# Performance work log

Hardware: AMD Instinct MI355X
Metric: run time of the kernel (lower is better)

## Reference

```python
import jax, jax.numpy as jnp
import numpy as np

H = 128  # hidden_size


def _cell(x_t, h, c, wih, whh, b):
    # PyTorch LSTM gate order: i, f, g, o
    z = x_t @ wih.T + h @ whh.T + b
    i, f, g, o = jnp.split(z, 4, axis=-1)
    c_new = jax.nn.sigmoid(f) * c + jax.nn.sigmoid(i) * jnp.tanh(g)
    h_new = jax.nn.sigmoid(o) * jnp.tanh(c_new)
    return h_new, c_new


def _layer(xs, wih_f, whh_f, b_f, wih_b, whh_b, b_b):
    # NOTE: faithful to the original per-timestep loop: both 'directions'
    # are stepped FORWARD in time (the backward cell never sees reversed input
    # because each nn.LSTM call has seq_len=1 with carried state).
    B = xs.shape[1]
    init = (jnp.zeros((B, H), xs.dtype), jnp.zeros((B, H), xs.dtype),
            jnp.zeros((B, H), xs.dtype), jnp.zeros((B, H), xs.dtype))

    def step(carry, x_t):
        hf, cf, hb, cb = carry
        hf, cf = _cell(x_t, hf, cf, wih_f, whh_f, b_f)
        hb, cb = _cell(x_t, hb, cb, wih_b, whh_b, b_b)
        return (hf, cf, hb, cb), jnp.concatenate([hf, hb], axis=-1)

    _, ys = jax.lax.scan(step, init, xs)
    return ys  # [S, B, 2H]


def setup_inputs() -> dict:
    key = jax.random.key(0)
    ks = jax.random.split(key, 16)
    S, B, D = 4096, 64, 96
    s = 0.05
    p = {
        'x': jax.random.normal(ks[0], (S, B, D), jnp.float32),
        # layer 0 (input D), forward + backward direction weights
        'wih0f': jax.random.normal(ks[1], (4 * H, D)) * s,
        'whh0f': jax.random.normal(ks[2], (4 * H, H)) * s,
        'b0f': jax.random.normal(ks[3], (4 * H,)) * s,
        'wih0b': jax.random.normal(ks[4], (4 * H, D)) * s,
        'whh0b': jax.random.normal(ks[5], (4 * H, H)) * s,
        'b0b': jax.random.normal(ks[6], (4 * H,)) * s,
        # layer 1 (input 2H)
        'wih1f': jax.random.normal(ks[7], (4 * H, 2 * H)) * s,
        'whh1f': jax.random.normal(ks[8], (4 * H, H)) * s,
        'b1f': jax.random.normal(ks[9], (4 * H,)) * s,
        'wih1b': jax.random.normal(ks[10], (4 * H, 2 * H)) * s,
        'whh1b': jax.random.normal(ks[11], (4 * H, H)) * s,
        'b1b': jax.random.normal(ks[12], (4 * H,)) * s,
        'fc_w': jax.random.normal(ks[13], (1, 2 * H)) * s,
        'fc_b': jax.random.normal(ks[14], (1,)) * s,
    }
    return p


def reference(x, wih0f, whh0f, b0f, wih0b, whh0b, b0b,
              wih1f, whh1f, b1f, wih1b, whh1b, b1b, fc_w, fc_b):
    ys = _layer(x, wih0f, whh0f, b0f, wih0b, whh0b, b0b)      # [S,B,2H]
    ys = _layer(ys, wih1f, whh1f, b1f, wih1b, whh1b, b1b)     # [S,B,2H]
    out = jax.nn.sigmoid(ys @ fc_w.T + fc_b)                  # [S,B,1]
    return out
```

## Files before the change

kernel.cpp:

```cpp
#include <hip/hip_runtime.h>
#include <stdint.h>

typedef short short8 __attribute__((ext_vector_type(8)));
typedef short short4v __attribute__((ext_vector_type(4)));
typedef float floatx4 __attribute__((ext_vector_type(4)));

#define LOG2E 1.44269504088896340736f

template <int N> struct IC { static constexpr int value = N; };

__device__ __forceinline__ float bf2f(unsigned short u) {
  unsigned v = ((unsigned)u) << 16;
  return __builtin_bit_cast(float, v);
}
__device__ __forceinline__ unsigned short f2bf(float f) {
  unsigned v = __builtin_bit_cast(unsigned, f);
  v += 0x7FFFu + ((v >> 16) & 1u);
  return (unsigned short)(v >> 16);
}
__device__ __forceinline__ float fast_exp2(float x) {
#if __has_builtin(__builtin_amdgcn_exp2f)
  return __builtin_amdgcn_exp2f(x);
#else
  return exp2f(x);
#endif
}
__device__ __forceinline__ float fast_rcp(float x) {
#if __has_builtin(__builtin_amdgcn_rcpf)
  return __builtin_amdgcn_rcpf(x);
#else
  return 1.0f / x;
#endif
}
__device__ __forceinline__ float fsig(float x) {
  return fast_rcp(1.0f + fast_exp2(-LOG2E * x));
}
__device__ __forceinline__ floatx4 mfma16(short8 a, short8 b, floatx4 c) {
  return __builtin_amdgcn_mfma_f32_16x16x32_bf16(a, b, c, 0, 0, 0);
}

__global__ __launch_bounds__(256) void detect_kernel(
    const unsigned short* __restrict__ w, int n_u16, int* __restrict__ flag)
{
  __shared__ int cnt;
  if (threadIdx.x == 0) cnt = 0;
  __syncthreads();
  int local = 0;
  for (int i = threadIdx.x * 2; i < n_u16; i += 512) {
    unsigned e = (w[i] >> 7) & 0xFF;
    if (e >= 0xF0) local++;
  }
  atomicAdd(&cnt, local);
  __syncthreads();
  if (threadIdx.x == 0) *flag = (cnt > 64) ? 1 : 0;
}

__global__ __launch_bounds__(256) void convertw_kernel(
    const void* s0, const void* s1, const void* s2, const void* s3,
    const void* s4, const void* s5, const void* s6, const void* s7,
    const void* s8, const void* s9, const void* s10, const void* s11,
    const void* s12, const void* s13,
    unsigned short* __restrict__ wbuf, const int* __restrict__ flag)
{
  const void* srcs[14] = {s0, s1, s2, s3, s4, s5, s6, s7, s8, s9, s10, s11, s12, s13};
  const int woff[14] = {0,      49152,  114688, 115200, 164352, 229888,
                        230400, 361472, 427008, 427520, 558592, 624128,
                        624640, 624896};
  const int wlen[14] = {49152, 65536, 512, 49152, 65536, 512,
                        131072, 65536, 512, 131072, 65536, 512, 256, 1};
  const int glen[14] = {96 * 128, 128 * 128, 128, 96 * 128, 128 * 128, 128,
                        256 * 128, 128 * 128, 128, 256 * 128, 128 * 128, 128,
                        0, 0};
  int sb = 0, i = 0;
  for (i = 0; i < 14; ++i) {
    int nb = (wlen[i] + 1023) >> 10;
    if ((int)blockIdx.x < sb + nb) break;
    sb += nb;
  }
  const int base = ((int)blockIdx.x - sb) * 1024 + (int)threadIdx.x * 4;
  unsigned short* dst = wbuf + woff[i];
  const int f32 = *flag;
  const int gl = glen[i];
#pragma unroll
  for (int j = 0; j < 4; ++j) {
    const int idx = base + j;
    if (idx >= wlen[i]) break;
    float v = f32 ? ((const float*)srcs[i])[idx]
                  : bf2f(((const unsigned short*)srcs[i])[idx]);
    if (gl) {
      const int gate = (int)((unsigned)idx / (unsigned)gl);
      v *= (gate == 2) ? (2.0f * LOG2E) : LOG2E;
    }
    dst[idx] = f2bf(v);
  }
}

template <int K>
__device__ __forceinline__ void gemm512_body(
    unsigned short* As, int t, int slice,
    const void* __restrict__ A, size_t a_off, int dyn,
    const int* __restrict__ flag,
    const unsigned short* __restrict__ Bf, const unsigned short* __restrict__ Bb,
    const unsigned short* __restrict__ biasf, const unsigned short* __restrict__ biasb,
    unsigned short* __restrict__ Z)
{
  constexpr int RS = K + 8;
  const int tid = threadIdx.x, lane = tid & 63;
  const int q = lane >> 4, cc = lane & 15;
  constexpr int K8 = K / 8;
  const int use32 = dyn ? *flag : 0;
  if (use32) {
    const float* Arow = (const float*)A + a_off + (size_t)t * 64 * K;
    for (int ci = tid; ci < 64 * K8; ci += 512) {
      int r_ = ci / K8, c8 = ci % K8;
      const float* p = Arow + r_ * K + c8 * 8;
      floatx4 x0 = *(const floatx4*)p;
      floatx4 x1 = *(const floatx4*)(p + 4);
      short8 s;
#pragma unroll
      for (int j = 0; j < 4; ++j) {
        s[j] = (short)f2bf(x0[j]);
        s[4 + j] = (short)f2bf(x1[j]);
      }
      *(short8*)&As[r_ * RS + c8 * 8] = s;
    }
  } else {
    const unsigned short* Arow = (const unsigned short*)A + a_off + (size_t)t * 64 * K;
    for (int ci = tid; ci < 64 * K8; ci += 512) {
      int r_ = ci / K8, c8 = ci % K8;
      *(short8*)&As[r_ * RS + c8 * 8] = *(const short8*)&Arow[r_ * K + c8 * 8];
    }
  }
  __syncthreads();
  const int w = tid >> 6;
  const unsigned short* Bp    = slice ? Bb : Bf;
  const unsigned short* biasp = slice ? biasb : biasf;
  const int cb = w * 64;
  const int dslab = slice * 4;
  floatx4 acc[4][4];
#pragma unroll
  for (int m = 0; m < 4; ++m)
#pragma unroll
    for (int n = 0; n < 4; ++n)
#pragma unroll
      for (int r = 0; r < 4; ++r) acc[m][n][r] = 0.f;
#pragma unroll
  for (int ks = 0; ks < K / 32; ++ks) {
    short8 af[4], bfr[4];
#pragma unroll
    for (int m = 0; m < 4; ++m)
      af[m] = *(const short8*)&As[(m * 16 + cc) * RS + ks * 32 + q * 8];
#pragma unroll
    for (int n = 0; n < 4; ++n)
      bfr[n] = *(const short8*)&Bp[(size_t)(cb + n * 16 + cc) * K + ks * 32 + q * 8];
#pragma unroll
    for (int m = 0; m < 4; ++m)
#pragma unroll
      for (int n = 0; n < 4; ++n)
        acc[m][n] = mfma16(af[m], bfr[n], acc[m][n]);
  }
#pragma unroll
  for (int n = 0; n < 4; ++n) {
    const int col = cb + n * 16 + cc;
    const float bv = bf2f(biasp[col]);
    const int g = col >> 7, uu = col & 127;
#pragma unroll
    for (int m = 0; m < 4; ++m) {
      unsigned short* zb =
          Z + ((size_t)t * 8 + dslab + m) * 8192 + uu * 16 + q * 4 + g;
#pragma unroll
      for (int r = 0; r < 4; ++r)
        zb[r * 2048] = f2bf(acc[m][n][r] + bv);
    }
  }
}

__device__ __forceinline__ void fc512_body(
    int idx, int steps, const unsigned short* __restrict__ ys1,
    const unsigned short* __restrict__ fcw, const unsigned short* __restrict__ fcb,
    void* __restrict__ out, size_t out_off, const int* __restrict__ flag)
{
  const int tid = threadIdx.x;
  const int w = tid >> 6, lane = tid & 63;
  const int t = idx * 2 + (w >> 2);
  if (t >= steps) return;
  const int w4 = w & 3;
  const int o = lane & 15, q = lane >> 4;
  const int b = w4 * 16 + o;
  const unsigned short* rp = ys1 + ((size_t)t * 64 + b) * 256 + q * 64;
  float s = 0.f;
#pragma unroll
  for (int j = 0; j < 16; ++j) {
    short4v v = *(const short4v*)(rp + j * 4);
    const unsigned short* wp = fcw + q * 64 + j * 4;
#pragma unroll
    for (int k = 0; k < 4; ++k) s += bf2f((unsigned short)v[k]) * bf2f(wp[k]);
  }
  s += __shfl_xor(s, 16, 64);
  s += __shfl_xor(s, 32, 64);
  if (q == 0) {
    const float v = fsig(s + bf2f(fcb[0]));
    const size_t oidx = out_off + (size_t)t * 64 + b;
    if (*flag) ((float*)out)[oidx] = v;
    else       ((unsigned short*)out)[oidx] = f2bf(v);
  }
}

__global__ __attribute__((amdgpu_waves_per_eu(2, 4))) __launch_bounds__(512)
void rec_kernel(
    const unsigned short* __restrict__ Za, const unsigned short* __restrict__ whhfa,
    const unsigned short* __restrict__ whhba,
    unsigned short* __restrict__ ysa, float* __restrict__ ca,
    unsigned short* __restrict__ ha, int inita, int acta,
    const unsigned short* __restrict__ Zb, const unsigned short* __restrict__ whhfb,
    const unsigned short* __restrict__ whhbb,
    unsigned short* __restrict__ ysb, float* __restrict__ cb_,
    unsigned short* __restrict__ hb, int initb, int actb,
    int steps,
    const void* __restrict__ x, size_t x_off, int do96, const int* __restrict__ flag,
    const unsigned short* __restrict__ wih0f, const unsigned short* __restrict__ wih0b,
    const unsigned short* __restrict__ b0f, const unsigned short* __restrict__ b0b,
    unsigned short* __restrict__ Z0n,
    const unsigned short* __restrict__ ys0g, int do256,
    const unsigned short* __restrict__ wih1f, const unsigned short* __restrict__ wih1b,
    const unsigned short* __restrict__ b1f, const unsigned short* __restrict__ b1b,
    unsigned short* __restrict__ Z1n,
    const unsigned short* __restrict__ fcsrc,
    const unsigned short* __restrict__ fcw, const unsigned short* __restrict__ fcb,
    void* __restrict__ out, size_t fc_off, int fcn)
{
  __shared__ __align__(16) unsigned char smem[34816];
  const int bx = blockIdx.x;
  const int g96n = steps * 2;

  if (bx >= 64) {
    const int wi = bx - 64;
    if (wi < g96n) {
      if (!do96) return;
      gemm512_body<96>((unsigned short*)smem, wi >> 1, wi & 1, x, x_off, 1,
                       flag, wih0f, wih0b, b0f, b0b, Z0n);
    } else if (wi < 2 * g96n) {
      if (!do256) return;
      const int idx = wi - g96n;
      gemm512_body<256>((unsigned short*)smem, idx >> 1, idx & 1, ys0g, 0, 0,
                        flag, wih1f, wih1b, b1f, b1b, Z1n);
    } else {
      if (fcn <= 0) return;
      fc512_body(wi - 2 * g96n, steps, fcsrc, fcw, fcb, out, fc_off, flag);
    }
    return;
  }

  const int blk = bx;
  const int ctx = blk >> 5;
  if (ctx == 0 ? !acta : !actb) return;
  const int tid = threadIdx.x;

  const unsigned short* Z;
  const unsigned short* whhF;
  const unsigned short* whhB;
  unsigned short* ys;
  float* cst;
  unsigned short* hst;
  int init;
  if (ctx == 0) {
    Z = Za; whhF = whhfa; whhB = whhba; ys = ysa; cst = ca; hst = ha; init = inita;
  } else {
    Z = Zb; whhF = whhfb; whhB = whhbb; ys = ysb; cst = cb_; hst = hb; init = initb;
  }
  const int d = (blk >> 4) & 1, bg = (blk >> 2) & 3, bh = blk & 3;
  const unsigned short* whh = d ? whhB : whhF;

  unsigned short (*hbuf)[16][136] = (unsigned short(*)[16][136])smem;

  const int w = tid >> 6, lane = tid & 63, q = lane >> 4, cc = lane & 15;
  const int u = w * 16 + cc;

  short8 bfrag[4][4];
#pragma unroll
  for (int g = 0; g < 4; ++g)
#pragma unroll
    for (int k = 0; k < 4; ++k)
      bfrag[g][k] = *(const short8*)(whh + (size_t)(g * 128 + u) * 128 + k * 32 + q * 8);

  const int prow = (tid >> 7) * 4 + bh;
  const int pcol = tid & 127;

  {
    unsigned* hz = (unsigned*)smem;
    for (int i = tid; i < 2 * 16 * 68; i += 512) hz[i] = 0u;
  }
  __syncthreads();

  float creg;
  if (init) {
    creg = 0.f;
  } else {
    creg = cst[(size_t)(d * 64 + bg * 16 + q * 4 + bh) * 128 + u];
    hbuf[0][prow][pcol] = hst[(size_t)(d * 64 + bg * 16 + prow) * 128 + pcol];
  }
  __syncthreads();

  const size_t zoff =
      (size_t)(d * 4 + bg) * 8192 + (size_t)bh * 2048 + u * 16 + q * 4;
  const unsigned short* zpA = Z + zoff;
  const unsigned short* zpB = Z + zoff + 65536;
  short4v zA = *(const short4v*)zpA;
  short4v zB = *(const short4v*)zpB;
  zpA += 131072;
  zpB += 131072;

  unsigned short* ysb_ = ys + (size_t)(bg * 16 + prow) * 256 + d * 128 + pcol;

  auto half_step = [&](auto bhc, short4v& zs, const unsigned short*& zp, int t,
                       int cur, int nxt) __attribute__((always_inline)) {
    constexpr int BH = decltype(bhc)::value;
    floatx4 acc[4];
#pragma unroll
    for (int g = 0; g < 4; ++g)
#pragma unroll
      for (int r = 0; r < 4; ++r)
        acc[g][r] = (r == BH) ? bf2f((unsigned short)zs[g]) : 0.f;
    zs = *(const short4v*)zp;
    zp += 131072;

    short8 af[4];
#pragma unroll
    for (int k = 0; k < 4; ++k)
      af[k] = *(const short8*)&hbuf[cur][cc][k * 32 + q * 8];
#pragma unroll
    for (int g = 0; g < 4; ++g)
#pragma unroll
      for (int k = 0; k < 4; ++k)
        acc[g] = mfma16(af[k], bfrag[g][k], acc[g]);

    {
      const float ei = fast_exp2(acc[0][BH]);
      const float ef = fast_exp2(acc[1][BH]);
      const float eg = fast_exp2(acc[2][BH]);
      const float a1 = 1.0f + ei, a2 = 1.0f + eg, a3 = 1.0f + ef;
      const float p12 = a1 * a2;
      const float rD = fast_rcp(p12 * a3);
      const float t2 = __builtin_fmaf(eg, 2.0f * LOG2E, -2.0f * LOG2E);
      const float it2 = ei * t2 * (a3 * rD);
      const float sf = ef * (p12 * rD);
      const float cs = __builtin_fmaf(sf, creg, it2);
      creg = cs;
      const float eo = fast_exp2(acc[3][BH]);
      const float ec = fast_exp2(fminf(cs, 88.0f));
      const float h = eo * (ec - 1.0f) * fast_rcp((1.0f + eo) * (1.0f + ec));
      hbuf[nxt][q * 4 + BH][u] = f2bf(h);
    }
    asm volatile("s_waitcnt lgkmcnt(0)\n\ts_barrier" ::: "memory");
    ysb_[(size_t)t * 16384] = hbuf[nxt][prow][pcol];
  };

  auto run = [&](auto bhc) __attribute__((always_inline)) {
    int t = 0;
    for (; t + 2 <= steps; t += 2) {
      half_step(bhc, zA, zpA, t, 0, 1);
      half_step(bhc, zB, zpB, t + 1, 1, 0);
    }
    if (t < steps)
      half_step(bhc, zA, zpA, t, 0, 1);
  };
  switch (bh) {
    case 0: run(IC<0>{}); break;
    case 1: run(IC<1>{}); break;
    case 2: run(IC<2>{}); break;
    default: run(IC<3>{}); break;
  }

  cst[(size_t)(d * 64 + bg * 16 + q * 4 + bh) * 128 + u] = creg;
  const int fin = steps & 1;
  hst[(size_t)(d * 64 + bg * 16 + prow) * 128 + pcol] = hbuf[fin][prow][pcol];
}

__global__ __attribute__((amdgpu_waves_per_eu(2, 4))) __launch_bounds__(512)
void g96_kernel(
    const void* __restrict__ x, size_t x_off, const int* __restrict__ flag,
    const unsigned short* __restrict__ Bf, const unsigned short* __restrict__ Bb,
    const unsigned short* __restrict__ biasf, const unsigned short* __restrict__ biasb,
    unsigned short* __restrict__ Z)
{
  __shared__ __align__(16) unsigned short As[64 * 104];
  gemm512_body<96>(As, blockIdx.x >> 1, blockIdx.x & 1, x, x_off, 1, flag,
                   Bf, Bb, biasf, biasb, Z);
}

__global__ __launch_bounds__(256) void fc_kernel(
    const unsigned short* __restrict__ ys,
    const unsigned short* __restrict__ fcw,
    const unsigned short* __restrict__ fcb,
    void* __restrict__ out, size_t out_off, int n,
    const int* __restrict__ flag)
{
  const int gw = (int)((blockIdx.x * 256 + threadIdx.x) >> 6);
  const int lane = threadIdx.x & 63;
  if (gw >= n) return;
  const unsigned short* rp = ys + (size_t)gw * 256 + lane * 4;
  float s = 0.f;
#pragma unroll
  for (int i = 0; i < 4; ++i) s += bf2f(rp[i]) * bf2f(fcw[lane * 4 + i]);
#pragma unroll
  for (int m = 32; m >= 1; m >>= 1) s += __shfl_xor(s, m, 64);
  if (lane == 0) {
    const float v = fsig(s + bf2f(fcb[0]));
    if (*flag) ((float*)out)[out_off + gw] = v;
    else       ((unsigned short*)out)[out_off + gw] = f2bf(v);
  }
}

extern "C" void kernel_launch(void* const* d_in, const int* in_sizes, int n_in,
                              void* d_out, int out_size, void* d_ws, size_t ws_size,
                              hipStream_t stream)
{
  (void)in_sizes; (void)n_in; (void)out_size;
  const int S = 4096;

  int* flag = (int*)d_ws;
  unsigned short* wbuf = (unsigned short*)((char*)d_ws + 256);
  static const int woff[14] = {0,      49152,  114688, 115200, 164352, 229888,
                               230400, 361472, 427008, 427520, 558592, 624128,
                               624640, 624896};
  const size_t wbuf_end = 256 + 1250304;

  int C = 1;
  for (int cand = 128; cand >= 1; cand >>= 1) {
    size_t need = (size_t)cand * 655360 + wbuf_end + 196608;
    if (need <= ws_size) { C = cand; break; }
  }
  unsigned short* base = (unsigned short*)((char*)d_ws + wbuf_end);
  unsigned short* Z0buf[2] = {base, base + (size_t)C * 65536};
  unsigned short* Z1buf[2] = {base + (size_t)2 * C * 65536, base + (size_t)3 * C * 65536};
  unsigned short* ys0buf[2] = {base + (size_t)4 * C * 65536,
                               base + (size_t)4 * C * 65536 + (size_t)C * 16384};
  unsigned short* ys1buf[2] = {base + (size_t)4 * C * 65536 + (size_t)2 * C * 16384,
                               base + (size_t)4 * C * 65536 + (size_t)3 * C * 16384};
  float* c0 = (float*)(base + (size_t)4 * C * 65536 + (size_t)4 * C * 16384);
  float* c1 = c0 + 16384;
  unsigned short* h0 = (unsigned short*)(c1 + 16384);
  unsigned short* h1 = h0 + 16384;

  const unsigned short* wih0f = wbuf + woff[0];
  const unsigned short* whh0f = wbuf + woff[1];
  const unsigned short* b0f   = wbuf + woff[2];
  const unsigned short* wih0b = wbuf + woff[3];
  const unsigned short* whh0b = wbuf + woff[4];
  const unsigned short* b0b   = wbuf + woff[5];
  const unsigned short* wih1f = wbuf + woff[6];
  const unsigned short* whh1f = wbuf + woff[7];
  const unsigned short* b1f   = wbuf + woff[8];
  const unsigned short* wih1b = wbuf + woff[9];
  const unsigned short* whh1b = wbuf + woff[10];
  const unsigned short* b1b   = wbuf + woff[11];
  const unsigned short* fcw   = wbuf + woff[12];
  const unsigned short* fcb   = wbuf + woff[13];

  detect_kernel<<<1, 256, 0, stream>>>((const unsigned short*)d_in[1], 49152, flag);
  convertw_kernel<<<614, 256, 0, stream>>>(
      d_in[1], d_in[2], d_in[3], d_in[4], d_in[5], d_in[6], d_in[7],
      d_in[8], d_in[9], d_in[10], d_in[11], d_in[12], d_in[13], d_in[14],
      wbuf, flag);

  const int nc = S / C;
  g96_kernel<<<C * 2, 512, 0, stream>>>(d_in[0], 0, flag,
                                        wih0f, wih0b, b0f, b0b, Z0buf[0]);

  const int GX = 64 + 4 * C + (C + 1) / 2;
  for (int c = 0; c <= nc + 1; ++c) {
    const int p = c & 1, pn = (c + 1) & 1;
    rec_kernel<<<GX, 512, 0, stream>>>(
        Z0buf[p], whh0f, whh0b, ys0buf[p], c0, h0, (c == 0) ? 1 : 0,
        (c <= nc - 1) ? 1 : 0,
        Z1buf[p], whh1f, whh1b, ys1buf[p], c1, h1, (c == 2) ? 1 : 0,
        (c >= 2) ? 1 : 0,
        C,
        d_in[0], (size_t)(c + 1) * C * 6144, (c <= nc - 2) ? 1 : 0, flag,
        wih0f, wih0b, b0f, b0b, Z0buf[pn],
        ys0buf[pn], (c >= 1 && c <= nc) ? 1 : 0, wih1f, wih1b, b1f, b1b, Z1buf[pn],
        ys1buf[pn], fcw, fcb, d_out,
        (c >= 3) ? (size_t)(c - 3) * C * 64 : 0, (c >= 3) ? C * 64 : 0);
  }
  fc_kernel<<<C * 16, 256, 0, stream>>>(ys1buf[(nc - 1) & 1], fcw, fcb, d_out,
                                        (size_t)(nc - 1) * C * 64, C * 64, flag);
}
```

Measured before the change: 2.503 ms.

## Interleave both layer recurrences inside one workgroup to share barriers

Each recurrent workgroup now steps both the layer-0 and the layer-1 recurrence at once, instead of giving each layer its own set of 32 workgroups. Two independent MFMA and activation chains sit between a single barrier per timestep, which is meant to hide latency and halve the recurrent block count. The per-bh template specialisation is dropped by always placing the precomputed input in accumulator lane 0 and using a fixed row layout in shared memory. In exchange, each block holds twice the weight registers and a longer per-step critical path. It also writes ys for a layer even when that layer is inactive, which risks overwriting buffers during pipeline warm-up and drain.

```diff
diff --git a/kernel.cpp b/kernel.cpp
--- a/kernel.cpp
+++ b/kernel.cpp
@@ -6,8 +6,6 @@
 typedef float floatx4 __attribute__((ext_vector_type(4)));
 
 #define LOG2E 1.44269504088896340736f
-
-template <int N> struct IC { static constexpr int value = N; };
 
 __device__ __forceinline__ float bf2f(unsigned short u) {
   unsigned v = ((unsigned)u) << 16;
@@ -233,8 +231,8 @@
   const int bx = blockIdx.x;
   const int g96n = steps * 2;
 
-  if (bx >= 64) {
-    const int wi = bx - 64;
+  if (bx >= 32) {
+    const int wi = bx - 32;
     if (wi < g96n) {
       if (!do96) return;
       gemm512_body<96>((unsigned short*)smem, wi >> 1, wi & 1, x, x_off, 1,
@@ -251,129 +249,149 @@
     return;
   }
 
-  const int blk = bx;
-  const int ctx = blk >> 5;
-  if (ctx == 0 ? !acta : !actb) return;
+  if (!acta && !actb) return;
   const int tid = threadIdx.x;
-
-  const unsigned short* Z;
-  const unsigned short* whhF;
-  const unsigned short* whhB;
-  unsigned short* ys;
-  float* cst;
-  unsigned short* hst;
-  int init;
-  if (ctx == 0) {
-    Z = Za; whhF = whhfa; whhB = whhba; ys = ysa; cst = ca; hst = ha; init = inita;
-  } else {
-    Z = Zb; whhF = whhfb; whhB = whhbb; ys = ysb; cst = cb_; hst = hb; init = initb;
-  }
-  const int d = (blk >> 4) & 1, bg = (blk >> 2) & 3, bh = blk & 3;
-  const unsigned short* whh = d ? whhB : whhF;
-
-  unsigned short (*hbuf)[16][136] = (unsigned short(*)[16][136])smem;
+  const int d = bx >> 4, bg = (bx >> 2) & 3, bh = bx & 3;
+
+  unsigned short (*hbA)[16][136] = (unsigned short(*)[16][136])smem;
+  unsigned short (*hbB)[16][136] = (unsigned short(*)[16][136])(smem + 8704);
 
   const int w = tid >> 6, lane = tid & 63, q = lane >> 4, cc = lane & 15;
   const int u = w * 16 + cc;
-
-  short8 bfrag[4][4];
+  const int trow = (tid >> 7) * 4;
+  const int prow = trow + bh;
+  const int pcol = tid & 127;
+
+  const unsigned short* whA = d ? whhba : whhfa;
+  const unsigned short* whB = d ? whhbb : whhfb;
+  short8 bfA[4][4], bfB[4][4];
 #pragma unroll
   for (int g = 0; g < 4; ++g)
 #pragma unroll
-    for (int k = 0; k < 4; ++k)
-      bfrag[g][k] = *(const short8*)(whh + (size_t)(g * 128 + u) * 128 + k * 32 + q * 8);
-
-  const int prow = (tid >> 7) * 4 + bh;
-  const int pcol = tid & 127;
+    for (int k = 0; k < 4; ++k) {
+      bfA[g][k] = *(const short8*)(whA + (size_t)(g * 128 + u) * 128 + k * 32 + q * 8);
+      bfB[g][k] = *(const short8*)(whB + (size_t)(g * 128 + u) * 128 + k * 32 + q * 8);
+    }
 
   {
     unsigned* hz = (unsigned*)smem;
-    for (int i = tid; i < 2 * 16 * 68; i += 512) hz[i] = 0u;
+    for (int i = tid; i < 4352; i += 512) hz[i] = 0u;
   }
   __syncthreads();
 
-  float creg;
-  if (init) {
-    creg = 0.f;
+  float cregA, cregB;
+  if (inita) {
+    cregA = 0.f;
   } else {
-    creg = cst[(size_t)(d * 64 + bg * 16 + q * 4 + bh) * 128 + u];
-    hbuf[0][prow][pcol] = hst[(size_t)(d * 64 + bg * 16 + prow) * 128 + pcol];
+    cregA = ca[(size_t)(d * 64 + bg * 16 + q * 4 + bh) * 128 + u];
+    hbA[0][trow][pcol] = ha[(size_t)(d * 64 + bg * 16 + prow) * 128 + pcol];
+  }
+  if (initb) {
+    cregB = 0.f;
+  } else {
+    cregB = cb_[(size_t)(d * 64 + bg * 16 + q * 4 + bh) * 128 + u];
+    hbB[0][trow][pcol] = hb[(size_t)(d * 64 + bg * 16 + prow) * 128 + pcol];
   }
   __syncthreads();
 
   const size_t zoff =
       (size_t)(d * 4 + bg) * 8192 + (size_t)bh * 2048 + u * 16 + q * 4;
-  const unsigned short* zpA = Z + zoff;
-  const unsigned short* zpB = Z + zoff + 65536;
-  short4v zA = *(const short4v*)zpA;
-  short4v zB = *(const short4v*)zpB;
-  zpA += 131072;
-  zpB += 131072;
-
-  unsigned short* ysb_ = ys + (size_t)(bg * 16 + prow) * 256 + d * 128 + pcol;
-
-  auto half_step = [&](auto bhc, short4v& zs, const unsigned short*& zp, int t,
-                       int cur, int nxt) __attribute__((always_inline)) {
-    constexpr int BH = decltype(bhc)::value;
-    floatx4 acc[4];
-#pragma unroll
-    for (int g = 0; g < 4; ++g)
-#pragma unroll
-      for (int r = 0; r < 4; ++r)
-        acc[g][r] = (r == BH) ? bf2f((unsigned short)zs[g]) : 0.f;
-    zs = *(const short4v*)zp;
-    zp += 131072;
-
-    short8 af[4];
-#pragma unroll
-    for (int k = 0; k < 4; ++k)
-      af[k] = *(const short8*)&hbuf[cur][cc][k * 32 + q * 8];
-#pragma unroll
-    for (int g = 0; g < 4; ++g)
-#pragma unroll
-      for (int k = 0; k < 4; ++k)
-        acc[g] = mfma16(af[k], bfrag[g][k], acc[g]);
+  const unsigned short* zpAa = Za + zoff;
+  const unsigned short* zpBa = Za + zoff + 65536;
+  const unsigned short* zpAb = Zb + zoff;
+  const unsigned short* zpBb = Zb + zoff + 65536;
+  short4v zAa = *(const short4v*)zpAa;
+  short4v zBa = *(const short4v*)zpBa;
+  short4v zAb = *(const short4v*)zpAb;
+  short4v zBb = *(const short4v*)zpBb;
+  zpAa += 131072; zpBa += 131072; zpAb += 131072; zpBb += 131072;
+
+  unsigned short* ysA_ = ysa + (size_t)(bg * 16 + prow) * 256 + d * 128 + pcol;
+  unsigned short* ysB_ = ysb + (size_t)(bg * 16 + prow) * 256 + d * 128 + pcol;
+
+  auto half_step = [&](short4v& za_, const unsigned short*& zpa_,
+                       short4v& zb_, const unsigned short*& zpb_,
+                       int t, int cur, int nxt) __attribute__((always_inline)) {
+    floatx4 accA[4], accB[4];
+#pragma unroll
+    for (int g = 0; g < 4; ++g) {
+      accA[g][0] = bf2f((unsigned short)za_[g]);
+      accA[g][1] = 0.f; accA[g][2] = 0.f; accA[g][3] = 0.f;
+      accB[g][0] = bf2f((unsigned short)zb_[g]);
+      accB[g][1] = 0.f; accB[g][2] = 0.f; accB[g][3] = 0.f;
+    }
+    za_ = *(const short4v*)zpa_; zpa_ += 131072;
+    zb_ = *(const short4v*)zpb_; zpb_ += 131072;
+
+#pragma unroll
+    for (int k = 0; k < 4; ++k) {
+      short8 afA = *(const short8*)&hbA[cur][cc][k * 32 + q * 8];
+#pragma unroll
+      for (int g = 0; g < 4; ++g) accA[g] = mfma16(afA, bfA[g][k], accA[g]);
+    }
+#pragma unroll
+    for (int k = 0; k < 4; ++k) {
+      short8 afB = *(const short8*)&hbB[cur][cc][k * 32 + q * 8];
+#pragma unroll
+      for (int g = 0; g < 4; ++g) accB[g] = mfma16(afB, bfB[g][k], accB[g]);
+    }
 
     {
-      const float ei = fast_exp2(acc[0][BH]);
-      const float ef = fast_exp2(acc[1][BH]);
-      const float eg = fast_exp2(acc[2][BH]);
+      const float ei = fast_exp2(accA[0][0]);
+      const float ef = fast_exp2(accA[1][0]);
+      const float eg = fast_exp2(accA[2][0]);
       const float a1 = 1.0f + ei, a2 = 1.0f + eg, a3 = 1.0f + ef;
       const float p12 = a1 * a2;
       const float rD = fast_rcp(p12 * a3);
       const float t2 = __builtin_fmaf(eg, 2.0f * LOG2E, -2.0f * LOG2E);
       const float it2 = ei * t2 * (a3 * rD);
       const float sf = ef * (p12 * rD);
-      const float cs = __builtin_fmaf(sf, creg, it2);
-      creg = cs;
-      const float eo = fast_exp2(acc[3][BH]);
+      const float cs = __builtin_fmaf(sf, cregA, it2);
+      cregA = cs;
+      const float eo = fast_exp2(accA[3][0]);
       const float ec = fast_exp2(fminf(cs, 88.0f));
       const float h = eo * (ec - 1.0f) * fast_rcp((1.0f + eo) * (1.0f + ec));
-      hbuf[nxt][q * 4 + BH][u] = f2bf(h);
+      hbA[nxt][q * 4][u] = f2bf(h);
+    }
+    {
+      const float ei = fast_exp2(accB[0][0]);
+      const float ef = fast_exp2(accB[1][0]);
+      const float eg = fast_exp2(accB[2][0]);
+      const float a1 = 1.0f + ei, a2 = 1.0f + eg, a3 = 1.0f + ef;
+      const float p12 = a1 * a2;
+      const float rD = fast_rcp(p12 * a3);
+      const float t2 = __builtin_fmaf(eg, 2.0f * LOG2E, -2.0f * LOG2E);
+      const float it2 = ei * t2 * (a3 * rD);
+      const float sf = ef * (p12 * rD);
+      const float cs = __builtin_fmaf(sf, cregB, it2);
+      cregB = cs;
+      const float eo = fast_exp2(accB[3][0]);
+      const float ec = fast_exp2(fminf(cs, 88.0f));
+      const float h = eo * (ec - 1.0f) * fast_rcp((1.0f + eo) * (1.0f + ec));
+      hbB[nxt][q * 4][u] = f2bf(h);
     }
     asm volatile("s_waitcnt lgkmcnt(0)\n\ts_barrier" ::: "memory");
-    ysb_[(size_t)t * 16384] = hbuf[nxt][prow][pcol];
+    ysA_[(size_t)t * 16384] = hbA[nxt][trow][pcol];
+    ysB_[(size_t)t * 16384] = hbB[nxt][trow][pcol];
   };
 
-  auto run = [&](auto bhc) __attribute__((always_inline)) {
-    int t = 0;
-    for (; t + 2 <= steps; t += 2) {
-      half_step(bhc, zA, zpA, t, 0, 1);
-      half_step(bhc, zB, zpB, t + 1, 1, 0);
-    }
-    if (t < steps)
-      half_step(bhc, zA, zpA, t, 0, 1);
-  };
-  switch (bh) {
-    case 0: run(IC<0>{}); break;
-    case 1: run(IC<1>{}); break;
-    case 2: run(IC<2>{}); break;
-    default: run(IC<3>{}); break;
-  }
-
-  cst[(size_t)(d * 64 + bg * 16 + q * 4 + bh) * 128 + u] = creg;
+  int t = 0;
+  for (; t + 2 <= steps; t += 2) {
+    half_step(zAa, zpAa, zAb, zpAb, t, 0, 1);
+    half_step(zBa, zpBa, zBb, zpBb, t + 1, 1, 0);
+  }
+  if (t < steps)
+    half_step(zAa, zpAa, zAb, zpAb, t, 0, 1);
+
   const int fin = steps & 1;
-  hst[(size_t)(d * 64 + bg * 16 + prow) * 128 + pcol] = hbuf[fin][prow][pcol];
+  if (acta) {
+    ca[(size_t)(d * 64 + bg * 16 + q * 4 + bh) * 128 + u] = cregA;
+    ha[(size_t)(d * 64 + bg * 16 + prow) * 128 + pcol] = hbA[fin][trow][pcol];
+  }
+  if (actb) {
+    cb_[(size_t)(d * 64 + bg * 16 + q * 4 + bh) * 128 + u] = cregB;
+    hb[(size_t)(d * 64 + bg * 16 + prow) * 128 + pcol] = hbB[fin][trow][pcol];
+  }
 }
 
 __global__ __attribute__((amdgpu_waves_per_eu(2, 4))) __launch_bounds__(512)
@@ -467,7 +485,7 @@
   g96_kernel<<<C * 2, 512, 0, stream>>>(d_in[0], 0, flag,
                                         wih0f, wih0b, b0f, b0b, Z0buf[0]);
 
-  const int GX = 64 + 4 * C + (C + 1) / 2;
+  const int GX = 32 + 4 * C + (C + 1) / 2;
   for (int c = 0; c <= nc + 1; ++c) {
     const int p = c & 1, pn = (c + 1) & 1;
     rec_kernel<<<GX, 512, 0, stream>>>(
```

Result: slower. 4.010 ms (+60.2%).
